# Performance work log

Hardware: AMD Instinct MI355X
Metric: run time of the kernel (lower is better)

## Reference

```python
import jax, jax.numpy as jnp
import numpy as np

# ---- static configuration (mirrors init_kwargs) ----
B, V, C, NH, HD = 1, 6, 256, 8, 32     # batch, views, embed, heads, head_dim
Z, L, P = 4, 4, 2                       # z-ref points, fmap levels, ref points
BEV_H, BEV_W = 80, 80
Q = BEV_H * BEV_W
IMG_H, IMG_W = 480, 800
LEVEL_SHAPES = [(60, 100), (30, 50), (15, 25), (8, 13)]
S = sum(h * w for h, w in LEVEL_SHAPES)
RES = 0.512
OFFSET_SCALE = 1.0
FF = 512


def layer_norm(x, g, b):
    m = jnp.mean(x, -1, keepdims=True)
    v = jnp.var(x, -1, keepdims=True)
    return (x - m) / jnp.sqrt(v + 1e-5) * g + b


def _bev_grid():
    xs = (jnp.arange(BEV_W) + 0.5) / BEV_W
    ys = (jnp.arange(BEV_H) + 0.5) / BEV_H
    gy, gx = jnp.meshgrid(ys, xs, indexing='ij')
    ref = jnp.stack([gx.reshape(-1), gy.reshape(-1)], -1)        # (Q,2) normalized xy
    world = (ref - 0.5) * jnp.array([BEV_W * RES, BEV_H * RES])  # (Q,2) ego-frame meters
    return ref, world


def deform_sample(value, H, W, loc):
    """Bilinear sampling. value: (N, H*W, NH, HD); loc: (N, Qn, NH, PP, 2) in [0,1].
    Returns (N, Qn, NH, PP, HD); out-of-bounds samples contribute zero."""
    v = jnp.moveaxis(value, 2, 1)                                # (N, NH, HW, HD)
    x = loc[..., 0] * W - 0.5
    y = loc[..., 1] * H - 0.5
    x0 = jnp.floor(x); y0 = jnp.floor(y)
    lx, ly = x - x0, y - y0
    x0 = x0.astype(jnp.int32); y0 = y0.astype(jnp.int32)
    gather = jax.vmap(jax.vmap(lambda vt, it: vt[it]))           # over (N, NH)
    def corner(xi, yi, w):
        ok = ((xi >= 0) & (xi < W) & (yi >= 0) & (yi < H)).astype(value.dtype)
        idx = jnp.clip(yi, 0, H - 1) * W + jnp.clip(xi, 0, W - 1)
        g = gather(v, jnp.moveaxis(idx, 2, 1))                   # (N,NH,Qn,PP,HD)
        return jnp.moveaxis(g, 1, 2) * (w * ok)[..., None]
    return (corner(x0, y0, (1 - lx) * (1 - ly)) + corner(x0 + 1, y0, lx * (1 - ly))
            + corner(x0, y0 + 1, (1 - lx) * ly) + corner(x0 + 1, y0 + 1, lx * ly))


def _forward(bev_queries, bev_histories, multiscale_fmaps, transition_matrices, z_refs,
             cam_proj_matrices, Wv_t, Woff_t, boff_t, Ww_t, bw_t, Wo_t, bo_t, ln1_g, ln1_b,
             Wv_s, Woff_s, boff_s, Ww_s, bw_s, Wo_s, bo_s, ln2_g, ln2_b,
             W1, b1, W2, b2, ln3_g, ln3_b):
    ref, world = _bev_grid()
    q = bev_queries
    # ---------- temporal self-attention (deformable over current + warped history) ----------
    vcur = (q @ Wv_t).reshape(B, Q, NH, HD)
    vhist = (bev_histories @ Wv_t).reshape(B, Q, NH, HD)
    off_t = (q @ Woff_t + boff_t).reshape(B, Q, NH, 2, P, 2) * OFFSET_SCALE
    w_t = jax.nn.softmax((q @ Ww_t + bw_t).reshape(B, Q, NH, 2 * P), -1).reshape(B, Q, NH, 2, P)
    ext = jnp.array([BEV_W * RES, BEV_H * RES], jnp.float32)
    wh = jnp.concatenate([world, jnp.ones((Q, 1), jnp.float32)], -1)     # (Q,3)
    warped = jnp.einsum('bij,qj->bqi', transition_matrices, wh)          # (B,Q,3)
    ref_hist = warped[..., :2] / warped[..., 2:3] / ext + 0.5            # (B,Q,2)
    norm_bev = jnp.array([BEV_W, BEV_H], jnp.float32)
    loc_c = ref[None, :, None, None, :] + off_t[:, :, :, 0] / norm_bev
    loc_h = ref_hist[:, :, None, None, :] + off_t[:, :, :, 1] / norm_bev
    s_c = deform_sample(vcur, BEV_H, BEV_W, loc_c)                       # (B,Q,NH,P,HD)
    s_h = deform_sample(vhist, BEV_H, BEV_W, loc_h)
    out_t = (jnp.einsum('bqhp,bqhpd->bqhd', w_t[:, :, :, 0], s_c)
             + jnp.einsum('bqhp,bqhpd->bqhd', w_t[:, :, :, 1], s_h))
    out1 = out_t.reshape(B, Q, C) @ Wo_t + bo_t
    out2 = layer_norm(out1 + q, ln1_g, ln1_b)
    # ---------- spatial cross-attention (multi-view multi-scale deformable) ----------
    val = (multiscale_fmaps @ Wv_s).reshape(B * V, S, NH, HD)
    pts = jnp.concatenate([
        jnp.broadcast_to(world[:, None, :], (Q, Z, 2)),
        jnp.broadcast_to(z_refs[None, :, None], (Q, Z, 1)),
        jnp.ones((Q, Z, 1), jnp.float32)], -1)                           # (Q,Z,4) homogeneous
    uvd = jnp.einsum('vij,qzj->vqzi', cam_proj_matrices, pts)            # (V,Q,Z,3)
    d = uvd[..., 2]
    un = uvd[..., 0] / jnp.maximum(d, 1e-5) / IMG_W
    vn = uvd[..., 1] / jnp.maximum(d, 1e-5) / IMG_H
    valid = ((d > 1e-5) & (un >= 0) & (un <= 1) & (vn >= 0) & (vn <= 1)).astype(q.dtype)
    refuv = jnp.stack([un, vn], -1)                                      # (V,Q,Z,2)
    off_s = (out2 @ Woff_s + boff_s).reshape(B, Q, NH, Z, L, P, 2) * OFFSET_SCALE
    w_s = jax.nn.softmax((out2 @ Ww_s + bw_s).reshape(B, Q, NH, Z * L * P), -1)
    w_s = w_s.reshape(B, Q, NH, Z, L, P)
    acc = jnp.zeros((B, Q, NH, HD), q.dtype)
    start = 0
    for l, (Hl, Wl) in enumerate(LEVEL_SHAPES):
        vl = val[:, start:start + Hl * Wl]
        start += Hl * Wl
        loc = (refuv[None, :, :, None, :, None, :]
               + off_s[:, None, :, :, :, l] / jnp.array([Wl, Hl], jnp.float32))
        loc = jnp.broadcast_to(loc, (B, V, Q, NH, Z, P, 2)).reshape(B * V, Q, NH, Z * P, 2)
        samp = deform_sample(vl, Hl, Wl, loc).reshape(B, V, Q, NH, Z, P, HD)
        wl = w_s[:, None, :, :, :, l] * valid[None, :, :, None, :, None]
        acc = acc + jnp.einsum('bvqhzp,bvqhzpd->bqhd', wl, samp)
    count = jnp.maximum(valid.sum((0, 2)), 1.0)                          # (Q,) hit count
    out3 = (acc / count[None, :, None, None]).reshape(B, Q, C) @ Wo_s + bo_s
    out4 = layer_norm(out3 + out2, ln2_g, ln2_b)
    # ---------- feed-forward ----------
    out5 = jax.nn.relu(out4 @ W1 + b1) @ W2 + b2
    return layer_norm(out5 + out4, ln3_g, ln3_b)


def setup_inputs() -> dict:
    key = jax.random.key(0)
    ks = iter(jax.random.split(key, 40))
    def rn(shape, s=1.0):
        return jax.random.normal(next(ks), shape, jnp.float32) * s
    sc = 1.0 / float(np.sqrt(C))
    inp = {}
    inp['bev_queries'] = rn((B, Q, C), 0.1)
    inp['bev_histories'] = rn((B, Q, C), 0.1)
    inp['multiscale_fmaps'] = rn((B, V, S, C), 0.1)
    th = 0.02
    T = np.array([[np.cos(th), -np.sin(th), 0.5],
                  [np.sin(th), np.cos(th), 0.1],
                  [0.0, 0.0, 1.0]], np.float32)
    inp['transition_matrices'] = jnp.tile(jnp.asarray(T)[None], (B, 1, 1))
    inp['z_refs'] = jnp.linspace(-5.0, 3.0, Z).astype(jnp.float32)
    K = np.array([[400.0, 0.0, IMG_W / 2], [0.0, 400.0, IMG_H / 2], [0.0, 0.0, 1.0]], np.float32)
    Ps = []
    for vi in range(V):
        a = 2 * np.pi * vi / V
        Rt = np.zeros((3, 4), np.float32)
        Rt[0, :3] = [-np.sin(a), np.cos(a), 0.0]   # camera right
        Rt[1, :3] = [0.0, 0.0, -1.0]               # camera down
        Rt[2, :3] = [np.cos(a), np.sin(a), 0.0]    # camera forward
        Ps.append(K @ Rt)
    inp['cam_proj_matrices'] = jnp.asarray(np.stack(Ps))
    # temporal self-attention params
    inp['Wv_t'] = rn((C, C), sc)
    inp['Woff_t'] = rn((C, NH * 2 * P * 2), sc * 0.1)
    inp['boff_t'] = jnp.zeros((NH * 2 * P * 2,), jnp.float32)
    inp['Ww_t'] = rn((C, NH * 2 * P), sc)
    inp['bw_t'] = jnp.zeros((NH * 2 * P,), jnp.float32)
    inp['Wo_t'] = rn((C, C), sc)
    inp['bo_t'] = jnp.zeros((C,), jnp.float32)
    inp['ln1_g'] = jnp.ones((C,), jnp.float32)
    inp['ln1_b'] = jnp.zeros((C,), jnp.float32)
    # spatial cross-attention params
    inp['Wv_s'] = rn((C, C), sc)
    inp['Woff_s'] = rn((C, NH * Z * L * P * 2), sc * 0.1)
    inp['boff_s'] = jnp.zeros((NH * Z * L * P * 2,), jnp.float32)
    inp['Ww_s'] = rn((C, NH * Z * L * P), sc)
    inp['bw_s'] = jnp.zeros((NH * Z * L * P,), jnp.float32)
    inp['Wo_s'] = rn((C, C), sc)
    inp['bo_s'] = jnp.zeros((C,), jnp.float32)
    inp['ln2_g'] = jnp.ones((C,), jnp.float32)
    inp['ln2_b'] = jnp.zeros((C,), jnp.float32)
    # FFN params
    inp['W1'] = rn((C, FF), sc)
    inp['b1'] = jnp.zeros((FF,), jnp.float32)
    inp['W2'] = rn((FF, C), 1.0 / float(np.sqrt(FF)))
    inp['b2'] = jnp.zeros((C,), jnp.float32)
    inp['ln3_g'] = jnp.ones((C,), jnp.float32)
    inp['ln3_b'] = jnp.zeros((C,), jnp.float32)
    # static shape descriptors (treated as compile-time constants)
    inp['bev_spatial_shape'] = np.array([[BEV_H, BEV_W]], np.int64)
    inp['multiscale_fmap_shapes'] = np.array(LEVEL_SHAPES, np.int64)
    inp['img_spatial_shape'] = np.array([[IMG_H, IMG_W]], np.int64)
    return inp


def reference(bev_queries, bev_histories, multiscale_fmaps, transition_matrices, z_refs,
              cam_proj_matrices, Wv_t, Woff_t, boff_t, Ww_t, bw_t, Wo_t, bo_t, ln1_g, ln1_b,
              Wv_s, Woff_s, boff_s, Ww_s, bw_s, Wo_s, bo_s, ln2_g, ln2_b,
              W1, b1, W2, b2, ln3_g, ln3_b,
              bev_spatial_shape, multiscale_fmap_shapes, img_spatial_shape):
    return _forward(bev_queries, bev_histories, multiscale_fmaps, transition_matrices, z_refs,
                    cam_proj_matrices, Wv_t, Woff_t, boff_t, Ww_t, bw_t, Wo_t, bo_t, ln1_g, ln1_b,
                    Wv_s, Woff_s, boff_s, Ww_s, bw_s, Wo_s, bo_s, ln2_g, ln2_b,
                    W1, b1, W2, b2, ln3_g, ln3_b)
```

## Files before the change

### kernel.cpp

```cpp
#include <hip/hip_runtime.h>
#include <hip/hip_bf16.h>
#include <hip/hip_fp16.h>

typedef unsigned short u16;
typedef unsigned int u32;
typedef __attribute__((ext_vector_type(8))) _Float16 f16x8;
typedef __attribute__((ext_vector_type(4))) float f32x4;

#define Q_N  6400
#define S_N  7979
#define BEV  80

__device__ __forceinline__ float f16tof(u16 u) {
    __half h; *(u16*)&h = u; return __half2float(h);
}
__device__ __forceinline__ u16 ftof16(float f) {
    __half h = __float2half(f); return *(u16*)&h;
}

template <int AIN, int RELU, int OUTMODE, int SM4, int SM32>
__device__ __forceinline__ void gemm_body(
    const void* __restrict__ A, const u16* __restrict__ WT,
    const float* __restrict__ bias, const float* __restrict__ bias2,
    void* __restrict__ Cout, int M, int N, int K, int bx, int by,
    u16* Ah, u16* Wh)
{
    const int tid  = threadIdx.x;
    const int lane = tid & 63;
    const int wave = tid >> 6;
    const int wm = (wave >> 1) * 32, wn = (wave & 1) * 64;
    const int m0 = by * 64, n0 = bx * 128;
    const int arow = tid >> 2, ak = (tid & 3) * 8;
    const int wrow = tid >> 1, wk = (tid & 1) * 16;
    const int fr = lane & 15, g = lane >> 4;

    f32x4 acc[8];
    #pragma unroll
    for (int i = 0; i < 8; ++i) acc[i] = (f32x4)(0.f);

    for (int k0 = 0; k0 < K; k0 += 32) {
        {
            const bool okr = (m0 + arow) < M;
            u16* dh = &Ah[arow * 40 + ak];
            if (AIN == 0) {
                const float* ap = (const float*)A + (size_t)(m0 + arow) * K + k0 + ak;
                float4 v0 = okr ? *(const float4*)(ap)     : make_float4(0.f, 0.f, 0.f, 0.f);
                float4 v1 = okr ? *(const float4*)(ap + 4) : make_float4(0.f, 0.f, 0.f, 0.f);
                u16 hb[8];
                hb[0] = ftof16(v0.x); hb[1] = ftof16(v0.y);
                hb[2] = ftof16(v0.z); hb[3] = ftof16(v0.w);
                hb[4] = ftof16(v1.x); hb[5] = ftof16(v1.y);
                hb[6] = ftof16(v1.z); hb[7] = ftof16(v1.w);
                *(ushort4*)(dh)     = *(ushort4*)&hb[0];
                *(ushort4*)(dh + 4) = *(ushort4*)&hb[4];
            } else {
                const u16* ap = (const u16*)A + (size_t)(m0 + arow) * K + k0 + ak;
                uint4 u = okr ? *(const uint4*)ap : make_uint4(0, 0, 0, 0);
                *(uint4*)dh = u;
            }
        }
        {
            const size_t wo = (size_t)(n0 + wrow) * K + k0 + wk;
            *(uint4*)&Wh[wrow * 40 + wk]     = *(const uint4*)(WT + wo);
            *(uint4*)&Wh[wrow * 40 + wk + 8] = *(const uint4*)(WT + wo + 8);
        }
        __syncthreads();
        f16x8 fah[2], fwh[4];
        #pragma unroll
        for (int i = 0; i < 2; ++i)
            fah[i] = *(const f16x8*)&Ah[(wm + i * 16 + fr) * 40 + g * 8];
        #pragma unroll
        for (int j = 0; j < 4; ++j)
            fwh[j] = *(const f16x8*)&Wh[(wn + j * 16 + fr) * 40 + g * 8];
        #pragma unroll
        for (int i = 0; i < 2; ++i)
            #pragma unroll
            for (int j = 0; j < 4; ++j)
                acc[i * 4 + j] = __builtin_amdgcn_mfma_f32_16x16x32_f16(fah[i], fwh[j], acc[i * 4 + j], 0, 0, 0);
        __syncthreads();
    }
    const int g4r = g * 4;
    float bv[4];
    #pragma unroll
    for (int j = 0; j < 4; ++j) {
        int col = n0 + wn + j * 16 + fr;
        if (bias2) bv[j] = (col < 512) ? bias[col] : bias2[col - 512];
        else       bv[j] = bias ? bias[col] : 0.f;
    }
    const bool do_sm32 = SM32 && ((n0 + wn) >= 512);
    const bool do_sm4  = SM4 && (wn == 64);
    #pragma unroll
    for (int i = 0; i < 2; ++i) {
        #pragma unroll
        for (int r = 0; r < 4; ++r) {
            const int row = m0 + wm + i * 16 + g4r + r;
            float v0 = acc[i * 4 + 0][r] + bv[0];
            float v1 = acc[i * 4 + 1][r] + bv[1];
            float v2 = acc[i * 4 + 2][r] + bv[2];
            float v3 = acc[i * 4 + 3][r] + bv[3];
            if (RELU) {
                v0 = fmaxf(v0, 0.f); v1 = fmaxf(v1, 0.f);
                v2 = fmaxf(v2, 0.f); v3 = fmaxf(v3, 0.f);
            }
            if (SM4 && do_sm4) {
                float m0q = fmaxf(v0, __shfl_xor(v0, 1));
                m0q = fmaxf(m0q, __shfl_xor(m0q, 2));
                float e0 = __expf(v0 - m0q);
                float s0 = e0 + __shfl_xor(e0, 1);
                s0 += __shfl_xor(s0, 2);
                v0 = e0 / s0;
                float m1q = fmaxf(v1, __shfl_xor(v1, 1));
                m1q = fmaxf(m1q, __shfl_xor(m1q, 2));
                float e1 = __expf(v1 - m1q);
                float s1 = e1 + __shfl_xor(e1, 1);
                s1 += __shfl_xor(s1, 2);
                v1 = e1 / s1;
                v2 = 0.f; v3 = 0.f;
            }
            if (SM32 && do_sm32) {
                float ma = fmaxf(v0, v1);
                ma = fmaxf(ma, __shfl_xor(ma, 1));
                ma = fmaxf(ma, __shfl_xor(ma, 2));
                ma = fmaxf(ma, __shfl_xor(ma, 4));
                ma = fmaxf(ma, __shfl_xor(ma, 8));
                float e0 = __expf(v0 - ma), e1 = __expf(v1 - ma);
                float sa = e0 + e1;
                sa += __shfl_xor(sa, 1);
                sa += __shfl_xor(sa, 2);
                sa += __shfl_xor(sa, 4);
                sa += __shfl_xor(sa, 8);
                float ia = 1.f / sa;
                v0 = e0 * ia; v1 = e1 * ia;
                float mb = fmaxf(v2, v3);
                mb = fmaxf(mb, __shfl_xor(mb, 1));
                mb = fmaxf(mb, __shfl_xor(mb, 2));
                mb = fmaxf(mb, __shfl_xor(mb, 4));
                mb = fmaxf(mb, __shfl_xor(mb, 8));
                float e2 = __expf(v2 - mb), e3 = __expf(v3 - mb);
                float sb = e2 + e3;
                sb += __shfl_xor(sb, 1);
                sb += __shfl_xor(sb, 2);
                sb += __shfl_xor(sb, 4);
                sb += __shfl_xor(sb, 8);
                float ib = 1.f / sb;
                v2 = e2 * ib; v3 = e3 * ib;
            }
            if (row < M) {
                const int colb = n0 + wn + fr;
                if (OUTMODE == 1) {
                    u16* cp = (u16*)Cout + (size_t)row * N;
                    cp[colb]      = ftof16(v0);
                    cp[colb + 16] = ftof16(v1);
                    cp[colb + 32] = ftof16(v2);
                    cp[colb + 48] = ftof16(v3);
                } else {
                    float* cp = (float*)Cout + (size_t)row * N;
                    cp[colb]      = v0;
                    cp[colb + 16] = v1;
                    cp[colb + 32] = v2;
                    cp[colb + 48] = v3;
                }
            }
        }
    }
}

template <int AIN, int RELU, int OUTMODE, int SM32>
__global__ __launch_bounds__(256) void mgemm_k(
    const void* __restrict__ A, const u16* __restrict__ WT,
    const float* __restrict__ bias, const float* __restrict__ bias2,
    void* __restrict__ Cout, int M, int N, int K)
{
    __shared__ u16 Ah[64 * 40], Wh[128 * 40];
    gemm_body<AIN, RELU, OUTMODE, 0, SM32>(A, WT, bias, bias2, Cout,
                                           M, N, K, blockIdx.x, blockIdx.y, Ah, Wh);
}

__global__ __launch_bounds__(256) void fused3_k(
    const float* __restrict__ fmaps, const float* __restrict__ q, const float* __restrict__ hist,
    const u16* __restrict__ Wv_s_h, const u16* __restrict__ Wv_t_h,
    const u16* __restrict__ Wc_h, const float* __restrict__ bc,
    u16* __restrict__ val_f16, u16* __restrict__ vcur, u16* __restrict__ vhist,
    float* __restrict__ owt)
{
    __shared__ u16 Ah[64 * 40], Wh[128 * 40];
    const int b = blockIdx.x;
    if (b < 1498) {
        gemm_body<0, 0, 1, 0, 0>(fmaps, Wv_s_h, nullptr, nullptr, val_f16,
                                 47874, 256, 256, b & 1, b >> 1, Ah, Wh);
    } else if (b < 1698) {
        int l = b - 1498;
        gemm_body<0, 0, 1, 0, 0>(q, Wv_t_h, nullptr, nullptr, vcur,
                                 6400, 256, 256, l & 1, l >> 1, Ah, Wh);
    } else if (b < 1898) {
        int l = b - 1698;
        gemm_body<0, 0, 1, 0, 0>(hist, Wv_t_h, nullptr, nullptr, vhist,
                                 6400, 256, 256, l & 1, l >> 1, Ah, Wh);
    } else {
        int l = b - 1898;
        gemm_body<0, 0, 0, 1, 0>(q, Wc_h, bc, nullptr, owt,
                                 6400, 128, 256, 0, l, Ah, Wh);
    }
}

__global__ __launch_bounds__(256) void wprep_k(
    const float* __restrict__ w0, const float* __restrict__ w1, const float* __restrict__ w2,
    const float* __restrict__ w3, const float* __restrict__ w4, const float* __restrict__ w5,
    const float* __restrict__ w6, const float* __restrict__ w7, u16* __restrict__ base,
    const float* __restrict__ Woff_t, const float* __restrict__ Ww_t,
    const float* __restrict__ boff_t, const float* __restrict__ bw_t,
    float* __restrict__ bc)
{
    const int b = blockIdx.x, tid = threadIdx.x;
    if (b == 184) {
        if (tid < 128) bc[tid] = (tid < 64) ? boff_t[tid] : (tid < 96 ? bw_t[tid - 64] : 0.f);
        return;
    }
    const int cum[10]  = {0, 16, 32, 48, 80, 96, 112, 144, 176, 184};
    const int Ks[9]    = {256, 256, 256, 256, 256, 256, 256, 512, 256};
    const int Ns[9]    = {256, 256, 256, 512, 256, 256, 512, 256, 128};
    const int hoff[9]  = {0, 65536, 131072, 196608, 327680, 393216, 458752, 589824, 720896};
    int seg = 0;
    #pragma unroll
    for (int s = 1; s < 9; ++s) if (b >= cum[s]) seg = s;
    const int K = Ks[seg], N = Ns[seg];
    const int t = b - cum[seg];
    const int ntn = N / 64;
    const int k0 = (t / ntn) * 64, n0 = (t % ntn) * 64;
    __shared__ float tile[64][65];
    const int rr = tid >> 2, cc = (tid & 3) * 16;
    if (seg < 8) {
        const float* W = seg == 0 ? w0 : seg == 1 ? w1 : seg == 2 ? w2 : seg == 3 ? w3 :
                         seg == 4 ? w4 : seg == 5 ? w5 : seg == 6 ? w6 : w7;
        #pragma unroll
        for (int c = 0; c < 4; ++c) {
            float4 v = *(const float4*)(W + (size_t)(k0 + rr) * N + n0 + cc + c * 4);
            tile[rr][cc + c * 4 + 0] = v.x;
            tile[rr][cc + c * 4 + 1] = v.y;
            tile[rr][cc + c * 4 + 2] = v.z;
            tile[rr][cc + c * 4 + 3] = v.w;
        }
    } else {
        #pragma unroll
        for (int i = 0; i < 16; ++i) {
            int n = n0 + cc + i, k = k0 + rr;
            float v = (n < 64) ? Woff_t[k * 64 + n] : (n < 96 ? Ww_t[k * 32 + n - 64] : 0.f);
            tile[rr][cc + i] = v;
        }
    }
    __syncthreads();
    const int nr = tid >> 2, kc = (tid & 3) * 16;
    u16 hb[16];
    #pragma unroll
    for (int i = 0; i < 16; ++i) hb[i] = ftof16(tile[kc + i][nr]);
    u16* hp = base + hoff[seg] + (size_t)(n0 + nr) * K + k0 + kc;
    *(ushort4*)(hp + 0)  = *(ushort4*)&hb[0];
    *(ushort4*)(hp + 4)  = *(ushort4*)&hb[4];
    *(ushort4*)(hp + 8)  = *(ushort4*)&hb[8];
    *(ushort4*)(hp + 12) = *(ushort4*)&hb[12];
}

__global__ __launch_bounds__(256) void ln_k(
    const float* __restrict__ x, const float* __restrict__ res,
    const float* __restrict__ g, const float* __restrict__ b,
    float* __restrict__ out)
{
    const int row = blockIdx.x, t = threadIdx.x;
    const size_t idx = (size_t)row * 256 + t;
    float v = x[idx] + res[idx];
    float s = v, ss = v * v;
    #pragma unroll
    for (int o = 32; o > 0; o >>= 1) {
        s += __shfl_down(s, o);
        ss += __shfl_down(ss, o);
    }
    __shared__ float red[8];
    __shared__ float mv[2];
    const int wv = t >> 6, ln = t & 63;
    if (ln == 0) { red[wv] = s; red[4 + wv] = ss; }
    __syncthreads();
    if (t == 0) {
        float S = red[0] + red[1] + red[2] + red[3];
        float SS = red[4] + red[5] + red[6] + red[7];
        float mean = S * (1.f / 256.f);
        float var = SS * (1.f / 256.f) - mean * mean;
        mv[0] = mean;
        mv[1] = rsqrtf(var + 1e-5f);
    }
    __syncthreads();
    out[idx] = (v - mv[0]) * mv[1] * g[t] + b[t];
}

__device__ __forceinline__ float4 bilin4h(const u16* __restrict__ v, int H, int W,
                                          float x, float y, int chb)
{
    float xf = floorf(x), yf = floorf(y);
    int x0 = (int)xf, y0 = (int)yf;
    int x1 = x0 + 1, y1 = y0 + 1;
    float fx = x - xf, fy = y - yf;
    float w00 = (1.f - fx) * (1.f - fy), w10 = fx * (1.f - fy);
    float w01 = (1.f - fx) * fy,         w11 = fx * fy;
    bool xi0 = (x0 >= 0) && (x0 < W);
    bool xi1 = (x1 >= 0) && (x1 < W);
    bool yi0 = (y0 >= 0) && (y0 < H);
    bool yi1 = (y1 >= 0) && (y1 < H);
    float4 r = make_float4(0.f, 0.f, 0.f, 0.f);
    #define CORNER(xi, yi, xx, yy, ww)                                           \
        if ((yi) && (xi)) {                                                      \
            uint2 u = *(const uint2*)(v + ((size_t)(yy) * W + (xx)) * 256 + chb);\
            float2 f0 = __half22float2(*(const __half2*)&u.x);                   \
            float2 f1 = __half22float2(*(const __half2*)&u.y);                   \
            r.x += (ww) * f0.x; r.y += (ww) * f0.y;                              \
            r.z += (ww) * f1.x; r.w += (ww) * f1.y;                              \
        }
    CORNER(xi0, yi0, x0, y0, w00)
    CORNER(xi1, yi0, x1, y0, w10)
    CORNER(xi0, yi1, x0, y1, w01)
    CORNER(xi1, yi1, x1, y1, w11)
    #undef CORNER
    return r;
}

__global__ __launch_bounds__(256) void temporal_k(
    const u16* __restrict__ vcur, const u16* __restrict__ vhist,
    const float* __restrict__ ow,
    const float* __restrict__ Tm, float* __restrict__ outt)
{
    const int b = blockIdx.x;
    const int q = (b & 7) * 800 + (b >> 3);
    const int tid = threadIdx.x;
    const int c4 = tid & 63, rep = tid >> 6;
    const int br = rep >> 1, p = rep & 1;
    const int h = c4 >> 3;
    const int chb = h * 32 + (c4 & 7) * 4;
    const int jx = q % BEV, iy = q / BEV;
    const float refx = (jx + 0.5f) / 80.f;
    const float refy = (iy + 0.5f) / 80.f;
    const float wx = (refx - 0.5f) * 40.96f;
    const float wy = (refy - 0.5f) * 40.96f;
    float bx, by;
    const u16* v;
    if (br == 0) { v = vcur; bx = refx; by = refy; }
    else {
        float h0 = Tm[0] * wx + Tm[1] * wy + Tm[2];
        float h1 = Tm[3] * wx + Tm[4] * wy + Tm[5];
        float h2 = Tm[6] * wx + Tm[7] * wy + Tm[8];
        v = vhist;
        bx = h0 / h2 / 40.96f + 0.5f;
        by = h1 / h2 / 40.96f + 0.5f;
    }
    const float* owq = ow + (size_t)q * 128;
    int ob = h * 8 + br * 4 + p * 2;
    float lx = bx + owq[ob] * (1.f / 80.f);
    float ly = by + owq[ob + 1] * (1.f / 80.f);
    float wgt = owq[64 + h * 4 + br * 2 + p];
    float4 sv = bilin4h(v, BEV, BEV, lx * 80.f - 0.5f, ly * 80.f - 0.5f, chb);
    __shared__ float4 s_acc[4][64];
    s_acc[rep][c4] = make_float4(wgt * sv.x, wgt * sv.y, wgt * sv.z, wgt * sv.w);
    __syncthreads();
    if (rep == 0) {
        float4 a = s_acc[0][c4], b2 = s_acc[1][c4], c = s_acc[2][c4], d = s_acc[3][c4];
        float4 o = make_float4(a.x + b2.x + c.x + d.x, a.y + b2.y + c.y + d.y,
                               a.z + b2.z + c.z + d.z, a.w + b2.w + c.w + d.w);
        *(float4*)(outt + (size_t)q * 256 + c4 * 4) = o;
    }
}

__global__ __launch_bounds__(256) void spatial_k(
    const u16* __restrict__ val, const u16* __restrict__ ow,
    const float* __restrict__ cam, const float* __restrict__ zrefs,
    float* __restrict__ out)
{
    const int b = blockIdx.x;
    const int q = (b & 7) * 800 + (b >> 3);
    const int tid = threadIdx.x;
    const int lane = tid & 63, wave = tid >> 6;
    const int hw = lane >> 5, lh = lane & 31;
    const int slot = wave * 2 + hw;
    const int h = lh >> 2, chb = h * 32 + (lh & 3) * 8;
    __shared__ float s_un[24], s_vn[24], s_ok[24];
    __shared__ int s_list[24];
    __shared__ int s_n;
    __shared__ float s_cnt;
    __shared__ float s_ox[256], s_oy[256], s_wt[256];
    __shared__ float s_part[8][256];
    const int jx = q % BEV, iy = q / BEV;
    const float wx = ((jx + 0.5f) / 80.f - 0.5f) * 40.96f;
    const float wy = ((iy + 0.5f) / 80.f - 0.5f) * 40.96f;
    if (tid < 24) {
        int v = tid >> 2, zz = tid & 3;
        float zr = zrefs[zz];
        const float* P = cam + v * 12;
        float u0 = P[0] * wx + P[1] * wy + P[2] * zr + P[3];
        float u1 = P[4] * wx + P[5] * wy + P[6] * zr + P[7];
        float dd = P[8] * wx + P[9] * wy + P[10] * zr + P[11];
        float dm = fmaxf(dd, 1e-5f);
        float un = u0 / dm / 800.f;
        float vn = u1 / dm / 480.f;
        bool ok = (dd > 1e-5f) && (un >= 0.f) && (un <= 1.f) && (vn >= 0.f) && (vn <= 1.f);
        s_un[tid] = un; s_vn[tid] = vn; s_ok[tid] = ok ? 1.f : 0.f;
    }
    {
        const u16* owq = ow + (size_t)q * 768;
        #pragma unroll
        for (int rep = 0; rep < 2; ++rep) {
            int flat = tid + rep * 256;
            int hh = flat >> 6, rem = flat & 63;
            int zz = rem >> 4, ll = (rem >> 2) & 3, pp = (rem >> 1) & 1, xy = rem & 1;
            int dst = (zz * 8 + ll * 2 + pp) * 8 + hh;
            float v = f16tof(owq[flat]);
            if (xy) s_oy[dst] = v; else s_ox[dst] = v;
        }
        int hh = tid >> 5, rem = tid & 31;
        s_wt[rem * 8 + hh] = f16tof(owq[512 + tid]);
    }
    __syncthreads();
    if (tid == 0) {
        int n = 0; float c = 0.f;
        for (int vz = 0; vz < 24; ++vz) {
            if (s_ok[vz] != 0.f) { s_list[n++] = vz; c += 1.f; }
        }
        s_n = n; s_cnt = fmaxf(c, 1.f);
    }
    __syncthreads();
    const int n = s_n;
    const int LH[4] = {60, 30, 15, 8};
    const int LW[4] = {100, 50, 25, 13};
    const int LS[4] = {0, 6000, 7500, 7875};
    float a0 = 0.f, a1 = 0.f, a2 = 0.f, a3 = 0.f, a4 = 0.f, a5 = 0.f, a6 = 0.f, a7 = 0.f;
    for (int it = slot; it < n; it += 8) {
        int vz = s_list[it];
        int v = vz >> 2, z = vz & 3;
        float un = s_un[vz], vn = s_vn[vz];
        #pragma unroll
        for (int l = 0; l < 4; ++l) {
            const int Hl = LH[l], Wl = LW[l];
            const u16* lv = val + ((size_t)v * S_N + LS[l]) * 256 + chb;
            const float unl = un * Wl - 0.5f, vnl = vn * Hl - 0.5f;
            #pragma unroll
            for (int p = 0; p < 2; ++p) {
                int idx = (z * 8 + l * 2 + p) * 8 + h;
                float x = unl + s_ox[idx];
                float y = vnl + s_oy[idx];
                float wgt = s_wt[idx];
                float xf = floorf(x), yf = floorf(y);
                int x0 = (int)xf, y0 = (int)yf;
                float fx = x - xf, fy = y - yf;
                __half2 w00 = __float2half2_rn((1.f - fx) * (1.f - fy) * wgt);
                __half2 w10 = __float2half2_rn(fx * (1.f - fy) * wgt);
                __half2 w01 = __float2half2_rn((1.f - fx) * fy * wgt);
                __half2 w11 = __float2half2_rn(fx * fy * wgt);
                bool xi0 = (x0 >= 0) && (x0 < Wl);
                bool xi1 = (x0 + 1 >= 0) && (x0 + 1 < Wl);
                bool yi0 = (y0 >= 0) && (y0 < Hl);
                bool yi1 = (y0 + 1 >= 0) && (y0 + 1 < Hl);
                const u16* r0p = lv + (size_t)y0 * (Wl * 256);
                const u16* r1p = r0p + (size_t)(Wl * 256);
                __half2 h0 = __float2half2_rn(0.f), h1 = h0, h2 = h0, h3 = h0;
                if (yi0 && xi0) {
                    uint4 u = *(const uint4*)(r0p + (size_t)x0 * 256);
                    const __half2* hp = (const __half2*)&u;
                    h0 = __hfma2(w00, hp[0], h0); h1 = __hfma2(w00, hp[1], h1);
                    h2 = __hfma2(w00, hp[2], h2); h3 = __hfma2(w00, hp[3], h3);
                }
                if (yi0 && xi1) {
                    uint4 u = *(const uint4*)(r0p + (size_t)(x0 + 1) * 256);
                    const __half2* hp = (const __half2*)&u;
                    h0 = __hfma2(w10, hp[0], h0); h1 = __hfma2(w10, hp[1], h1);
                    h2 = __hfma2(w10, hp[2], h2); h3 = __hfma2(w10, hp[3], h3);
                }
                if (yi1 && xi0) {
                    uint4 u = *(const uint4*)(r1p + (size_t)x0 * 256);
                    const __half2* hp = (const __half2*)&u;
                    h0 = __hfma2(w01, hp[0], h0); h1 = __hfma2(w01, hp[1], h1);
                    h2 = __hfma2(w01, hp[2], h2); h3 = __hfma2(w01, hp[3], h3);
                }
                if (yi1 && xi1) {
                    uint4 u = *(const uint4*)(r1p + (size_t)(x0 + 1) * 256);
                    const __half2* hp = (const __half2*)&u;
                    h0 = __hfma2(w11, hp[0], h0); h1 = __hfma2(w11, hp[1], h1);
                    h2 = __hfma2(w11, hp[2], h2); h3 = __hfma2(w11, hp[3], h3);
                }
                float2 f0 = __half22float2(h0), f1 = __half22float2(h1);
                float2 f2 = __half22float2(h2), f3 = __half22float2(h3);
                a0 += f0.x; a1 += f0.y; a2 += f1.x; a3 += f1.y;
                a4 += f2.x; a5 += f2.y; a6 += f3.x; a7 += f3.y;
            }
        }
    }
    *(float4*)&s_part[slot][chb]     = make_float4(a0, a1, a2, a3);
    *(float4*)&s_part[slot][chb + 4] = make_float4(a4, a5, a6, a7);
    __syncthreads();
    float sum = 0.f;
    #pragma unroll
    for (int k = 0; k < 8; ++k) sum += s_part[k][tid];
    out[(size_t)q * 256 + tid] = sum / s_cnt;
}

extern "C" void kernel_launch(void* const* d_in, const int* in_sizes, int n_in,
                              void* d_out, int out_size, void* d_ws, size_t ws_size,
                              hipStream_t stream) {
    (void)in_sizes; (void)n_in; (void)out_size; (void)ws_size;
    const float* q      = (const float*)d_in[0];
    const float* hist   = (const float*)d_in[1];
    const float* fmaps  = (const float*)d_in[2];
    const float* Tm     = (const float*)d_in[3];
    const float* zrefs  = (const float*)d_in[4];
    const float* cam    = (const float*)d_in[5];
    const float* Woff_t = (const float*)d_in[7];
    const float* boff_t = (const float*)d_in[8];
    const float* Ww_t   = (const float*)d_in[9];
    const float* bw_t   = (const float*)d_in[10];
    const float* bo_t   = (const float*)d_in[12];
    const float* ln1g   = (const float*)d_in[13];
    const float* ln1b   = (const float*)d_in[14];
    const float* boff_s = (const float*)d_in[17];
    const float* bw_s   = (const float*)d_in[19];
    const float* bo_s   = (const float*)d_in[21];
    const float* ln2g   = (const float*)d_in[22];
    const float* ln2b   = (const float*)d_in[23];
    const float* b1     = (const float*)d_in[25];
    const float* b2     = (const float*)d_in[27];
    const float* ln3g   = (const float*)d_in[28];
    const float* ln3b   = (const float*)d_in[29];

    float* ws    = (float*)d_ws;
    float* r0    = ws;
    float* r1    = ws + 1638400;
    float* owt   = ws + 3276800;
    float* r4    = ws + 4096000;
    u16*  r5u    = (u16*)(ws + 5734400);
    float* of4   = ws + 8192000;
    u16*  valbuf = (u16*)(ws + 9830400);
    u16*  vcur   = (u16*)(ws + 15958272);
    u16*  vhist  = (u16*)(ws + 16777472);
    u16*  wtab   = (u16*)(ws + 17596672);
    float* bc    = ws + 18350336;

    u16* hidden = valbuf;
    u16* Wv_t_h = wtab + 0;
    u16* Wo_t_h = wtab + 65536;
    u16* Wv_s_h = wtab + 131072;
    u16* Comb_h = wtab + 196608;
    u16* Wo_s_h = wtab + 393216;
    u16* W1_h   = wtab + 458752;
    u16* W2_h   = wtab + 589824;
    u16* Wc_h   = wtab + 720896;

    dim3 blk(256);
    auto gm = [](int M, int N) { return dim3((unsigned)(N / 128), (unsigned)((M + 63) / 64)); };

    wprep_k<<<dim3(185), blk, 0, stream>>>(
        (const float*)d_in[6], (const float*)d_in[11], (const float*)d_in[15],
        (const float*)d_in[16], (const float*)d_in[18], (const float*)d_in[20],
        (const float*)d_in[24], (const float*)d_in[26], wtab,
        Woff_t, Ww_t, boff_t, bw_t, bc);
    fused3_k<<<dim3(1998), blk, 0, stream>>>(
        fmaps, q, hist, Wv_s_h, Wv_t_h, Wc_h, bc,
        valbuf, vcur, vhist, owt);
    temporal_k<<<dim3(6400), blk, 0, stream>>>(vcur, vhist, owt, Tm, r4);
    mgemm_k<0,0,0,0><<<gm(6400, 256), blk, 0, stream>>>(
        r4, Wo_t_h, bo_t, nullptr, r0, 6400, 256, 256);
    ln_k<<<dim3(6400), blk, 0, stream>>>(r0, q, ln1g, ln1b, r1);
    mgemm_k<0,0,1,1><<<gm(6400, 768), blk, 0, stream>>>(
        r1, Comb_h, boff_s, bw_s, r5u, 6400, 768, 256);
    spatial_k<<<dim3(6400), blk, 0, stream>>>(valbuf, r5u, cam, zrefs, r0);
    mgemm_k<0,0,0,0><<<gm(6400, 256), blk, 0, stream>>>(
        r0, Wo_s_h, bo_s, nullptr, r4, 6400, 256, 256);
    ln_k<<<dim3(6400), blk, 0, stream>>>(r4, r1, ln2g, ln2b, of4);
    mgemm_k<0,1,1,0><<<gm(6400, 512), blk, 0, stream>>>(
        of4, W1_h, b1, nullptr, hidden, 6400, 512, 256);
    mgemm_k<1,0,0,0><<<gm(6400, 256), blk, 0, stream>>>(
        hidden, W2_h, b2, nullptr, r0, 6400, 256, 512);
    ln_k<<<dim3(6400), blk, 0, stream>>>(r0, of4, ln3g, ln3b, (float*)d_out);
}
```

Baseline: 326.1 us.

## Add small-tile full-K GEMM kernel and flatten spatial sampling loop branchlessly

Replaces the 64x128 tiled GEMM used for the post-attention projections and FFN with a new 32x64-tile kernel. It stages the whole 256-wide K slice into shared memory in one step, which gives more blocks per GEMM and fewer barriers per K step. The spatial deformable-sampling loop now spreads work across (view/z, level) pairs instead of only view/z. It also replaces the per-corner branches with clamped, always-executed loads whose weights are masked to zero. The trade-offs are a larger shared-memory footprint and less reuse per tile in the GEMMs, plus extra loads for out-of-bounds corners in sampling.

Result: slower. 360.4 us (+10.5%).

```diff
diff --git a/kernel.cpp b/kernel.cpp
--- a/kernel.cpp
+++ b/kernel.cpp
@@ -87,7 +87,6 @@
         if (bias2) bv[j] = (col < 512) ? bias[col] : bias2[col - 512];
         else       bv[j] = bias ? bias[col] : 0.f;
     }
-    const bool do_sm32 = SM32 && ((n0 + wn) >= 512);
     const bool do_sm4  = SM4 && (wn == 64);
     #pragma unroll
     for (int i = 0; i < 2; ++i) {
@@ -116,34 +115,6 @@
                 s1 += __shfl_xor(s1, 2);
                 v1 = e1 / s1;
                 v2 = 0.f; v3 = 0.f;
-            }
-            if (SM32 && do_sm32) {
-                float ma = fmaxf(v0, v1);
-                ma = fmaxf(ma, __shfl_xor(ma, 1));
-                ma = fmaxf(ma, __shfl_xor(ma, 2));
-                ma = fmaxf(ma, __shfl_xor(ma, 4));
-                ma = fmaxf(ma, __shfl_xor(ma, 8));
-                float e0 = __expf(v0 - ma), e1 = __expf(v1 - ma);
-                float sa = e0 + e1;
-                sa += __shfl_xor(sa, 1);
-                sa += __shfl_xor(sa, 2);
-                sa += __shfl_xor(sa, 4);
-                sa += __shfl_xor(sa, 8);
-                float ia = 1.f / sa;
-                v0 = e0 * ia; v1 = e1 * ia;
-                float mb = fmaxf(v2, v3);
-                mb = fmaxf(mb, __shfl_xor(mb, 1));
-                mb = fmaxf(mb, __shfl_xor(mb, 2));
-                mb = fmaxf(mb, __shfl_xor(mb, 4));
-                mb = fmaxf(mb, __shfl_xor(mb, 8));
-                float e2 = __expf(v2 - mb), e3 = __expf(v3 - mb);
-                float sb = e2 + e3;
-                sb += __shfl_xor(sb, 1);
-                sb += __shfl_xor(sb, 2);
-                sb += __shfl_xor(sb, 4);
-                sb += __shfl_xor(sb, 8);
-                float ib = 1.f / sb;
-                v2 = e2 * ib; v3 = e3 * ib;
             }
             if (row < M) {
                 const int colb = n0 + wn + fr;
@@ -163,17 +134,6 @@
             }
         }
     }
-}
-
-template <int AIN, int RELU, int OUTMODE, int SM32>
-__global__ __launch_bounds__(256) void mgemm_k(
-    const void* __restrict__ A, const u16* __restrict__ WT,
-    const float* __restrict__ bias, const float* __restrict__ bias2,
-    void* __restrict__ Cout, int M, int N, int K)
-{
-    __shared__ u16 Ah[64 * 40], Wh[128 * 40];
-    gemm_body<AIN, RELU, OUTMODE, 0, SM32>(A, WT, bias, bias2, Cout,
-                                           M, N, K, blockIdx.x, blockIdx.y, Ah, Wh);
 }
 
 __global__ __launch_bounds__(256) void fused3_k(
@@ -200,6 +160,136 @@
         int l = b - 1898;
         gemm_body<0, 0, 0, 1, 0>(q, Wc_h, bc, nullptr, owt,
                                  6400, 128, 256, 0, l, Ah, Wh);
+    }
+}
+
+template <int AIN, int RELU, int OUTMODE, int SM4, int SM32>
+__global__ __launch_bounds__(256, 2) void sgemm_k(
+    const void* __restrict__ A, const u16* __restrict__ WT,
+    const float* __restrict__ bias, const float* __restrict__ bias2,
+    void* __restrict__ Cout, int M, int N, int K)
+{
+    __shared__ u16 Ah[8][1288];
+    __shared__ u16 Wh[8][2568];
+    const int tid  = threadIdx.x;
+    const int lane = tid & 63;
+    const int wave = tid >> 6;
+    const int wm = (wave >> 1) * 16, wn = (wave & 1) * 32;
+    const int m0 = blockIdx.y * 32, n0 = blockIdx.x * 64;
+    const int fr = lane & 15, g = lane >> 4;
+
+    const int ar  = tid >> 3, cch = tid & 7;
+    const int wrow = tid >> 2, wc4 = tid & 3;
+
+    f32x4 acc[2] = {(f32x4)(0.f), (f32x4)(0.f)};
+
+    for (int k0 = 0; k0 < K; k0 += 256) {
+        if (k0) __syncthreads();
+        {
+            const bool okr = (m0 + ar) < M;
+            u16 hb[32];
+            if (AIN == 0) {
+                const float* ap = (const float*)A + (size_t)(m0 + ar) * K + k0 + cch * 32;
+                #pragma unroll
+                for (int i = 0; i < 8; ++i) {
+                    float4 v = okr ? *(const float4*)(ap + i * 4) : make_float4(0.f, 0.f, 0.f, 0.f);
+                    hb[i * 4 + 0] = ftof16(v.x); hb[i * 4 + 1] = ftof16(v.y);
+                    hb[i * 4 + 2] = ftof16(v.z); hb[i * 4 + 3] = ftof16(v.w);
+                }
+            } else {
+                const u16* ap = (const u16*)A + (size_t)(m0 + ar) * K + k0 + cch * 32;
+                #pragma unroll
+                for (int i = 0; i < 4; ++i)
+                    *(uint4*)&hb[i * 8] = okr ? *(const uint4*)(ap + i * 8) : make_uint4(0, 0, 0, 0);
+            }
+            u16* dst = &Ah[cch][ar * 40];
+            #pragma unroll
+            for (int i = 0; i < 8; ++i)
+                *(ushort4*)(dst + i * 4) = *(ushort4*)&hb[i * 4];
+        }
+        {
+            const size_t wo = (size_t)(n0 + wrow) * K + k0 + wc4 * 64;
+            #pragma unroll
+            for (int half = 0; half < 2; ++half) {
+                u16* dst = &Wh[wc4 * 2 + half][wrow * 40];
+                const u16* src = WT + wo + half * 32;
+                #pragma unroll
+                for (int i = 0; i < 4; ++i)
+                    *(uint4*)(dst + i * 8) = *(const uint4*)(src + i * 8);
+            }
+        }
+        __syncthreads();
+        #pragma unroll
+        for (int c = 0; c < 8; ++c) {
+            f16x8 fa  = *(const f16x8*)&Ah[c][(wm + fr) * 40 + g * 8];
+            f16x8 fw0 = *(const f16x8*)&Wh[c][(wn + fr) * 40 + g * 8];
+            f16x8 fw1 = *(const f16x8*)&Wh[c][(wn + 16 + fr) * 40 + g * 8];
+            acc[0] = __builtin_amdgcn_mfma_f32_16x16x32_f16(fa, fw0, acc[0], 0, 0, 0);
+            acc[1] = __builtin_amdgcn_mfma_f32_16x16x32_f16(fa, fw1, acc[1], 0, 0, 0);
+        }
+    }
+    const int g4r = g * 4;
+    const int c0g = n0 + wn + fr, c1g = c0g + 16;
+    float bv0, bv1;
+    if (bias2) {
+        bv0 = (c0g < 512) ? bias[c0g] : bias2[c0g - 512];
+        bv1 = (c1g < 512) ? bias[c1g] : bias2[c1g - 512];
+    } else {
+        bv0 = bias ? bias[c0g] : 0.f;
+        bv1 = bias ? bias[c1g] : 0.f;
+    }
+    const bool do_sm32 = SM32 && ((n0 + wn) >= 512);
+    const bool do_sm4  = SM4 && ((n0 + wn) == 64);
+    const bool zr4     = SM4 && ((n0 + wn) == 96);
+    #pragma unroll
+    for (int r = 0; r < 4; ++r) {
+        const int row = m0 + wm + g4r + r;
+        float v0 = acc[0][r] + bv0;
+        float v1 = acc[1][r] + bv1;
+        if (RELU) { v0 = fmaxf(v0, 0.f); v1 = fmaxf(v1, 0.f); }
+        if (SM4) {
+            if (do_sm4) {
+                float m0q = fmaxf(v0, __shfl_xor(v0, 1));
+                m0q = fmaxf(m0q, __shfl_xor(m0q, 2));
+                float e0 = __expf(v0 - m0q);
+                float s0 = e0 + __shfl_xor(e0, 1);
+                s0 += __shfl_xor(s0, 2);
+                v0 = e0 / s0;
+                float m1q = fmaxf(v1, __shfl_xor(v1, 1));
+                m1q = fmaxf(m1q, __shfl_xor(m1q, 2));
+                float e1 = __expf(v1 - m1q);
+                float s1 = e1 + __shfl_xor(e1, 1);
+                s1 += __shfl_xor(s1, 2);
+                v1 = e1 / s1;
+            }
+            if (zr4) { v0 = 0.f; v1 = 0.f; }
+        }
+        if (SM32 && do_sm32) {
+            float ma = fmaxf(v0, v1);
+            ma = fmaxf(ma, __shfl_xor(ma, 1));
+            ma = fmaxf(ma, __shfl_xor(ma, 2));
+            ma = fmaxf(ma, __shfl_xor(ma, 4));
+            ma = fmaxf(ma, __shfl_xor(ma, 8));
+            float e0 = __expf(v0 - ma), e1 = __expf(v1 - ma);
+            float sa = e0 + e1;
+            sa += __shfl_xor(sa, 1);
+            sa += __shfl_xor(sa, 2);
+            sa += __shfl_xor(sa, 4);
+            sa += __shfl_xor(sa, 8);
+            float ia = 1.f / sa;
+            v0 = e0 * ia; v1 = e1 * ia;
+        }
+        if (row < M) {
+            if (OUTMODE == 1) {
+                u16* cp = (u16*)Cout + (size_t)row * N;
+                cp[c0g] = ftof16(v0);
+                cp[c1g] = ftof16(v1);
+            } else {
+                float* cp = (float*)Cout + (size_t)row * N;
+                cp[c0g] = v0;
+                cp[c1g] = v1;
+            }
+        }
     }
 }
 
@@ -423,69 +513,75 @@
         s_n = n; s_cnt = fmaxf(c, 1.f);
     }
     __syncthreads();
-    const int n = s_n;
-    const int LH[4] = {60, 30, 15, 8};
-    const int LW[4] = {100, 50, 25, 13};
-    const int LS[4] = {0, 6000, 7500, 7875};
+    const int n4 = s_n * 4;
     float a0 = 0.f, a1 = 0.f, a2 = 0.f, a3 = 0.f, a4 = 0.f, a5 = 0.f, a6 = 0.f, a7 = 0.f;
-    for (int it = slot; it < n; it += 8) {
-        int vz = s_list[it];
-        int v = vz >> 2, z = vz & 3;
-        float un = s_un[vz], vn = s_vn[vz];
-        #pragma unroll
-        for (int l = 0; l < 4; ++l) {
-            const int Hl = LH[l], Wl = LW[l];
-            const u16* lv = val + ((size_t)v * S_N + LS[l]) * 256 + chb;
-            const float unl = un * Wl - 0.5f, vnl = vn * Hl - 0.5f;
-            #pragma unroll
-            for (int p = 0; p < 2; ++p) {
-                int idx = (z * 8 + l * 2 + p) * 8 + h;
-                float x = unl + s_ox[idx];
-                float y = vnl + s_oy[idx];
-                float wgt = s_wt[idx];
-                float xf = floorf(x), yf = floorf(y);
-                int x0 = (int)xf, y0 = (int)yf;
-                float fx = x - xf, fy = y - yf;
-                __half2 w00 = __float2half2_rn((1.f - fx) * (1.f - fy) * wgt);
-                __half2 w10 = __float2half2_rn(fx * (1.f - fy) * wgt);
-                __half2 w01 = __float2half2_rn((1.f - fx) * fy * wgt);
-                __half2 w11 = __float2half2_rn(fx * fy * wgt);
-                bool xi0 = (x0 >= 0) && (x0 < Wl);
-                bool xi1 = (x0 + 1 >= 0) && (x0 + 1 < Wl);
-                bool yi0 = (y0 >= 0) && (y0 < Hl);
-                bool yi1 = (y0 + 1 >= 0) && (y0 + 1 < Hl);
-                const u16* r0p = lv + (size_t)y0 * (Wl * 256);
-                const u16* r1p = r0p + (size_t)(Wl * 256);
-                __half2 h0 = __float2half2_rn(0.f), h1 = h0, h2 = h0, h3 = h0;
-                if (yi0 && xi0) {
-                    uint4 u = *(const uint4*)(r0p + (size_t)x0 * 256);
-                    const __half2* hp = (const __half2*)&u;
-                    h0 = __hfma2(w00, hp[0], h0); h1 = __hfma2(w00, hp[1], h1);
-                    h2 = __hfma2(w00, hp[2], h2); h3 = __hfma2(w00, hp[3], h3);
-                }
-                if (yi0 && xi1) {
-                    uint4 u = *(const uint4*)(r0p + (size_t)(x0 + 1) * 256);
-                    const __half2* hp = (const __half2*)&u;
-                    h0 = __hfma2(w10, hp[0], h0); h1 = __hfma2(w10, hp[1], h1);
-                    h2 = __hfma2(w10, hp[2], h2); h3 = __hfma2(w10, hp[3], h3);
-                }
-                if (yi1 && xi0) {
-                    uint4 u = *(const uint4*)(r1p + (size_t)x0 * 256);
-                    const __half2* hp = (const __half2*)&u;
-                    h0 = __hfma2(w01, hp[0], h0); h1 = __hfma2(w01, hp[1], h1);
-                    h2 = __hfma2(w01, hp[2], h2); h3 = __hfma2(w01, hp[3], h3);
-                }
-                if (yi1 && xi1) {
-                    uint4 u = *(const uint4*)(r1p + (size_t)(x0 + 1) * 256);
-                    const __half2* hp = (const __half2*)&u;
-                    h0 = __hfma2(w11, hp[0], h0); h1 = __hfma2(w11, hp[1], h1);
-                    h2 = __hfma2(w11, hp[2], h2); h3 = __hfma2(w11, hp[3], h3);
-                }
-                float2 f0 = __half22float2(h0), f1 = __half22float2(h1);
-                float2 f2 = __half22float2(h2), f3 = __half22float2(h3);
-                a0 += f0.x; a1 += f0.y; a2 += f1.x; a3 += f1.y;
-                a4 += f2.x; a5 += f2.y; a6 += f3.x; a7 += f3.y;
-            }
+    for (int w = slot; w < n4; w += 8) {
+        const int it = w >> 2, l = w & 3;
+        const int vz = s_list[it];
+        const int v = vz >> 2, z = vz & 3;
+        const float un = s_un[vz], vn = s_vn[vz];
+        const int Hl  = (l == 0) ? 60  : (l == 1) ? 30   : (l == 2) ? 15   : 8;
+        const int Wl  = (l == 0) ? 100 : (l == 1) ? 50   : (l == 2) ? 25   : 13;
+        const int LSo = (l == 0) ? 0   : (l == 1) ? 6000 : (l == 2) ? 7500 : 7875;
+        const u16* lv = val + ((size_t)v * S_N + LSo) * 256 + chb;
+        const float unl = un * Wl - 0.5f, vnl = vn * Hl - 0.5f;
+        const int Ws = Wl * 256;
+        #pragma unroll
+        for (int p = 0; p < 2; ++p) {
+            const int idx = (z * 8 + l * 2 + p) * 8 + h;
+            float x = unl + s_ox[idx];
+            float y = vnl + s_oy[idx];
+            float wgt = s_wt[idx];
+            float xf = floorf(x), yf = floorf(y);
+            int x0 = (int)xf, y0 = (int)yf;
+            float fx = x - xf, fy = y - yf;
+            bool xi0 = (x0 >= 0) & (x0 < Wl);
+            bool xi1 = (x0 >= -1) & (x0 < Wl - 1);
+            bool yi0 = (y0 >= 0) & (y0 < Hl);
+            bool yi1 = (y0 >= -1) & (y0 < Hl - 1);
+            int xc0 = min(max(x0, 0), Wl - 1);
+            int xc1 = min(max(x0 + 1, 0), Wl - 1);
+            int yc0 = min(max(y0, 0), Hl - 1);
+            int yc1 = min(max(y0 + 1, 0), Hl - 1);
+            float m00 = (xi0 & yi0) ? wgt : 0.f;
+            float m10 = (xi1 & yi0) ? wgt : 0.f;
+            float m01 = (xi0 & yi1) ? wgt : 0.f;
+            float m11 = (xi1 & yi1) ? wgt : 0.f;
+            __half2 w00 = __float2half2_rn((1.f - fx) * (1.f - fy) * m00);
+            __half2 w10 = __float2half2_rn(fx * (1.f - fy) * m10);
+            __half2 w01 = __float2half2_rn((1.f - fx) * fy * m01);
+            __half2 w11 = __float2half2_rn(fx * fy * m11);
+            const u16* r0p = lv + (size_t)yc0 * Ws;
+            const u16* r1p = lv + (size_t)yc1 * Ws;
+            uint4 u00 = *(const uint4*)(r0p + (size_t)xc0 * 256);
+            uint4 u10 = *(const uint4*)(r0p + (size_t)xc1 * 256);
+            uint4 u01 = *(const uint4*)(r1p + (size_t)xc0 * 256);
+            uint4 u11 = *(const uint4*)(r1p + (size_t)xc1 * 256);
+            __half2 h0 = __float2half2_rn(0.f), h1 = h0, h2 = h0, h3 = h0;
+            {
+                const __half2* hp = (const __half2*)&u00;
+                h0 = __hfma2(w00, hp[0], h0); h1 = __hfma2(w00, hp[1], h1);
+                h2 = __hfma2(w00, hp[2], h2); h3 = __hfma2(w00, hp[3], h3);
+            }
+            {
+                const __half2* hp = (const __half2*)&u10;
+                h0 = __hfma2(w10, hp[0], h0); h1 = __hfma2(w10, hp[1], h1);
+                h2 = __hfma2(w10, hp[2], h2); h3 = __hfma2(w10, hp[3], h3);
+            }
+            {
+                const __half2* hp = (const __half2*)&u01;
+                h0 = __hfma2(w01, hp[0], h0); h1 = __hfma2(w01, hp[1], h1);
+                h2 = __hfma2(w01, hp[2], h2); h3 = __hfma2(w01, hp[3], h3);
+            }
+            {
+                const __half2* hp = (const __half2*)&u11;
+                h0 = __hfma2(w11, hp[0], h0); h1 = __hfma2(w11, hp[1], h1);
+                h2 = __hfma2(w11, hp[2], h2); h3 = __hfma2(w11, hp[3], h3);
+            }
+            float2 f0 = __half22float2(h0), f1 = __half22float2(h1);
+            float2 f2 = __half22float2(h2), f3 = __half22float2(h3);
+            a0 += f0.x; a1 += f0.y; a2 += f1.x; a3 += f1.y;
+            a4 += f2.x; a5 += f2.y; a6 += f3.x; a7 += f3.y;
         }
     }
     *(float4*)&s_part[slot][chb]     = make_float4(a0, a1, a2, a3);
@@ -548,7 +644,7 @@
     u16* Wc_h   = wtab + 720896;
 
     dim3 blk(256);
-    auto gm = [](int M, int N) { return dim3((unsigned)(N / 128), (unsigned)((M + 63) / 64)); };
+    auto gs = [](int M, int N) { return dim3((unsigned)(N / 64), (unsigned)((M + 31) / 32)); };
 
     wprep_k<<<dim3(185), blk, 0, stream>>>(
         (const float*)d_in[6], (const float*)d_in[11], (const float*)d_in[15],
@@ -559,18 +655,18 @@
         fmaps, q, hist, Wv_s_h, Wv_t_h, Wc_h, bc,
         valbuf, vcur, vhist, owt);
     temporal_k<<<dim3(6400), blk, 0, stream>>>(vcur, vhist, owt, Tm, r4);
-    mgemm_k<0,0,0,0><<<gm(6400, 256), blk, 0, stream>>>(
+    sgemm_k<0,0,0,0,0><<<gs(6400, 256), blk, 0, stream>>>(
         r4, Wo_t_h, bo_t, nullptr, r0, 6400, 256, 256);
     ln_k<<<dim3(6400), blk, 0, stream>>>(r0, q, ln1g, ln1b, r1);
-    mgemm_k<0,0,1,1><<<gm(6400, 768), blk, 0, stream>>>(
+    sgemm_k<0,0,1,0,1><<<gs(6400, 768), blk, 0, stream>>>(
         r1, Comb_h, boff_s, bw_s, r5u, 6400, 768, 256);
     spatial_k<<<dim3(6400), blk, 0, stream>>>(valbuf, r5u, cam, zrefs, r0);
-    mgemm_k<0,0,0,0><<<gm(6400, 256), blk, 0, stream>>>(
+    sgemm_k<0,0,0,0,0><<<gs(6400, 256), blk, 0, stream>>>(
         r0, Wo_s_h, bo_s, nullptr, r4, 6400, 256, 256);
     ln_k<<<dim3(6400), blk, 0, stream>>>(r4, r1, ln2g, ln2b, of4);
-    mgemm_k<0,1,1,0><<<gm(6400, 512), blk, 0, stream>>>(
+    sgemm_k<0,1,1,0,0><<<gs(6400, 512), blk, 0, stream>>>(
         of4, W1_h, b1, nullptr, hidden, 6400, 512, 256);
-    mgemm_k<1,0,0,0><<<gm(6400, 256), blk, 0, stream>>>(
+    sgemm_k<1,0,0,0,0><<<gs(6400, 256), blk, 0, stream>>>(
         hidden, W2_h, b2, nullptr, r0, 6400, 256, 512);
     ln_k<<<dim3(6400), blk, 0, stream>>>(r0, of4, ln3g, ln3b, (float*)d_out);
 }
```
